# Performance work log

Measured on AMD Instinct MI355X. Metric: run time of the kernel, lower is better.

Reference implementation:

```python
import jax, jax.numpy as jnp
import numpy as np

N, E, D, H, ED = 50000, 150000, 128, 4, 16


def _ln(x, g, b, eps=1e-5):
    m = jnp.mean(x, -1, keepdims=True)
    v = jnp.var(x, -1, keepdims=True)
    return (x - m) / jnp.sqrt(v + eps) * g + b


def _seg_softmax(logits, seg, n):
    # numerically stable softmax over edges grouped by destination node
    m = jax.ops.segment_max(logits, seg, num_segments=n)
    e = jnp.exp(logits - m[seg])
    s = jax.ops.segment_sum(e, seg, num_segments=n)
    return e / (s[seg] + 1e-16)


def setup_inputs():
    key = jax.random.key(0)
    ks = jax.random.split(key, 16)
    def w(i, shape, s=0.05):
        return jax.random.normal(ks[i], shape, jnp.float32) * s
    return dict(
        x=w(0, (N, D), 1.0),
        edge_index=jax.random.randint(ks[1], (2, E), 0, N),
        edge_attr=w(2, (E, ED), 1.0),
        sage_Wl=w(3, (D, D)), sage_Wr=w(4, (D, D)), sage_b=jnp.zeros((D,), jnp.float32),
        tq_W=w(5, (D, H * D)), tq_b=jnp.zeros((H * D,), jnp.float32),
        tk_W=w(6, (D, H * D)), tk_b=jnp.zeros((H * D,), jnp.float32),
        tv_W=w(7, (D, H * D)), tv_b=jnp.zeros((H * D,), jnp.float32),
        te_W=w(8, (ED, H * D)),
        tskip_W=w(9, (D, D)), tskip_b=jnp.zeros((D,), jnp.float32),
        gat_W=w(10, (D, H * D)), gat_att_src=w(11, (H, D)), gat_att_dst=w(12, (H, D)),
        gat_bias=jnp.zeros((D,), jnp.float32),
        gate_short=jnp.ones((1,), jnp.float32), gate_attn=jnp.ones((1,), jnp.float32),
        gate_neighbor=jnp.ones((1,), jnp.float32),
        fus_W=w(13, (3 * D, D)), fus_b=jnp.zeros((D,), jnp.float32),
        fus_g=jnp.ones((D,), jnp.float32), fus_beta=jnp.zeros((D,), jnp.float32),
        norm_g=jnp.ones((D,), jnp.float32), norm_b=jnp.zeros((D,), jnp.float32),
    )


def reference(x, edge_index, edge_attr, sage_Wl, sage_Wr, sage_b,
              tq_W, tq_b, tk_W, tk_b, tv_W, tv_b, te_W, tskip_W, tskip_b,
              gat_W, gat_att_src, gat_att_dst, gat_bias,
              gate_short, gate_attn, gate_neighbor,
              fus_W, fus_b, fus_g, fus_beta, norm_g, norm_b):
    n, d = x.shape
    h = tq_W.shape[1] // d
    src, dst = edge_index[0], edge_index[1]

    # --- SAGEConv: mean aggregation of neighbors + root linear ---
    agg = jax.ops.segment_sum(x[src], dst, num_segments=n)
    cnt = jax.ops.segment_sum(jnp.ones((src.shape[0],), x.dtype), dst, num_segments=n)
    mean = agg / jnp.maximum(cnt, 1.0)[:, None]
    x_short = jax.nn.relu(mean @ sage_Wl + x @ sage_Wr + sage_b)

    # --- TransformerConv (concat=False, edge-conditioned key/value, skip) ---
    q = (x @ tq_W + tq_b).reshape(n, h, d)
    k = (x @ tk_W + tk_b).reshape(n, h, d)
    v = (x @ tv_W + tv_b).reshape(n, h, d)
    e = (edge_attr @ te_W).reshape(-1, h, d)           # [E,H,d]
    logits = jnp.sum(q[dst] * (k[src] + e), -1) / np.float32(np.sqrt(d))  # [E,H]
    alpha = _seg_softmax(logits, dst, n)
    out_t = jax.ops.segment_sum((v[src] + e) * alpha[..., None], dst, num_segments=n).mean(1)
    x_attn = jax.nn.relu(out_t + x @ tskip_W + tskip_b)

    # --- GATConv (adds self-loops, concat=False averages heads, bias) ---
    loops = jnp.arange(n)
    s2 = jnp.concatenate([src, loops])
    d2 = jnp.concatenate([dst, loops])
    g = (x @ gat_W).reshape(n, h, d)
    a_s = jnp.sum(g * gat_att_src, -1)                 # [N,H]
    a_d = jnp.sum(g * gat_att_dst, -1)
    lg = jax.nn.leaky_relu(a_s[s2] + a_d[d2], 0.2)     # [E+N,H]
    al = _seg_softmax(lg, d2, n)
    out_g = jax.ops.segment_sum(g[s2] * al[..., None], d2, num_segments=n).mean(1) + gat_bias
    x_nb = jax.nn.relu(out_g)

    # --- gated fusion + residual LayerNorm ---
    gs = jax.nn.sigmoid(gate_short)
    ga = jax.nn.sigmoid(gate_attn)
    gn = jax.nn.sigmoid(gate_neighbor)
    cat = jnp.concatenate([x_short * gs, x_attn * ga, x_nb * gn], -1)
    fused = jax.nn.relu(_ln(cat @ fus_W + fus_b, fus_g, fus_beta))
    return _ln(x + fused, norm_g, norm_b)
```

## Files before the change

kernel.cpp:

```cpp
#include <hip/hip_runtime.h>
#include <hip/hip_bf16.h>

using bf16 = __hip_bfloat16;
typedef __attribute__((ext_vector_type(8))) short short8;
typedef __attribute__((ext_vector_type(4))) float f32x4;
typedef __attribute__((ext_vector_type(4))) unsigned short u16x4;

__device__ __forceinline__ void store4(bf16* p, float v0, float v1, float v2, float v3) {
    u16x4 pk;
    bf16 h0 = __float2bfloat16(v0); pk[0] = *(unsigned short*)&h0;
    bf16 h1 = __float2bfloat16(v1); pk[1] = *(unsigned short*)&h1;
    bf16 h2 = __float2bfloat16(v2); pk[2] = *(unsigned short*)&h2;
    bf16 h3 = __float2bfloat16(v3); pk[3] = *(unsigned short*)&h3;
    *(u16x4*)p = pk;
}
__device__ __forceinline__ float b2f(short s) { bf16 h; *(short*)&h = s; return __bfloat162float(h); }

__global__ __launch_bounds__(256) void zero_ws(unsigned* p, size_t n) {
    size_t i = (size_t)blockIdx.x * 256 + threadIdx.x;
    size_t stride = (size_t)gridDim.x * 256;
    for (; i < n; i += stride) p[i] = 0u;
}

__global__ __launch_bounds__(256) void prep_all(
    const float* __restrict__ x, bf16* __restrict__ x_b,
    bf16* __restrict__ Wt_sage, const float* __restrict__ sage_Wl, const float* __restrict__ sage_Wr,
    bf16* __restrict__ Wt_fus, const float* __restrict__ fus_W,
    const float* __restrict__ gate_s, const float* __restrict__ gate_a, const float* __restrict__ gate_n,
    bf16* __restrict__ Wt_cat, const float* __restrict__ tvW,
    const float* __restrict__ tskipW, const float* __restrict__ teW,
    bf16* __restrict__ Wgag, const float* __restrict__ gatW,
    float* __restrict__ bvsum, const float* __restrict__ tvb, int ND)
{
    const int TP = 128 * 128;
    long i = (long)blockIdx.x * 256 + threadIdx.x;
    long nv = ND >> 3;
    if (i < nv) {
        long b = i * 8;
        f32x4 a0 = *(const f32x4*)(x + b);
        f32x4 a1 = *(const f32x4*)(x + b + 4);
        short8 o;
        #pragma unroll
        for (int j = 0; j < 4; ++j) { bf16 h = __float2bfloat16(a0[j]); o[j] = *(short*)&h; }
        #pragma unroll
        for (int j = 0; j < 4; ++j) { bf16 h = __float2bfloat16(a1[j]); o[4 + j] = *(short*)&h; }
        *(short8*)(x_b + b) = o;
        return;
    }
    i -= nv;
    if (i < TP) { int k = (int)i / 128, c = (int)i % 128; Wt_sage[c * 256 + k] = __float2bfloat16(sage_Wl[i]); return; }
    i -= TP;
    if (i < TP) { int k = (int)i / 128, c = (int)i % 128; Wt_sage[c * 256 + 128 + k] = __float2bfloat16(sage_Wr[i]); return; }
    i -= TP;
    if (i < 3 * TP) {
        int sseg = (int)(i / TP); int r = (int)(i % TP);
        int k = r / 128, c = r % 128;
        const float* g = sseg == 0 ? gate_s : (sseg == 1 ? gate_a : gate_n);
        float gv = 1.0f / (1.0f + expf(-g[0]));
        Wt_fus[c * 384 + sseg * 128 + k] = __float2bfloat16(fus_W[(size_t)sseg * TP + r] * gv);
        return;
    }
    i -= 3L * TP;
    if (i < 128L * 704) {
        int d = (int)(i / 704), kk = (int)(i % 704);
        float v;
        if (kk < 512)      { int h = kk >> 7, k = kk & 127; v = 0.25f * tvW[k * 512 + h * 128 + d]; }
        else if (kk < 640) { int k = kk - 512;              v = tskipW[k * 128 + d]; }
        else               { int t = kk - 640; int h = t >> 4, j = t & 15; v = 0.25f * teW[j * 512 + h * 128 + d]; }
        Wt_cat[(size_t)d * 704 + kk] = __float2bfloat16(v);
        return;
    }
    i -= 128L * 704;
    if (i < 128L * 512) {
        int d = (int)i >> 9, k = (int)i & 511;
        int h = k >> 7, i2 = k & 127;
        Wgag[i] = __float2bfloat16(0.25f * gatW[(size_t)i2 * 512 + h * 128 + d]);
        return;
    }
    i -= 128L * 512;
    if (i < 128) {
        int d = (int)i;
        bvsum[d] = 0.25f * (tvb[d] + tvb[128 + d] + tvb[256 + d] + tvb[384 + d]);
    }
}

__global__ __launch_bounds__(128) void build_wbig(
    bf16* __restrict__ Wbig, float* __restrict__ bbig,
    const float* __restrict__ Wq, const float* __restrict__ Wk,
    const float* __restrict__ teW, const float* __restrict__ bq,
    const float* __restrict__ bk, const float* __restrict__ gatW,
    const float* __restrict__ attS, const float* __restrict__ attD)
{
    int c = blockIdx.x;
    int ip = threadIdx.x;
    float acc = 0.f, bacc = 0.f;
    if (c < 512) {
        int h = c >> 7, i2 = c & 127;
        const float* wkrow = Wk + (size_t)i2 * 512 + h * 128;
        const float* wqrow = Wq + (size_t)ip * 512 + h * 128;
        for (int o = 0; o < 128; ++o) acc += wqrow[o] * wkrow[o];
        if (ip == 0) { const float* bqr = bq + h * 128; for (int o = 0; o < 128; ++o) bacc += bqr[o] * wkrow[o]; }
    } else if (c < 576) {
        int t = c - 512; int h = t >> 4, j = t & 15;
        const float* terow = teW + (size_t)j * 512 + h * 128;
        const float* wqrow = Wq + (size_t)ip * 512 + h * 128;
        for (int o = 0; o < 128; ++o) acc += wqrow[o] * terow[o];
        if (ip == 0) { const float* bqr = bq + h * 128; for (int o = 0; o < 128; ++o) bacc += bqr[o] * terow[o]; }
    } else if (c < 580) {
        int h = c - 576;
        const float* bkr = bk + h * 128;
        const float* wqrow = Wq + (size_t)ip * 512 + h * 128;
        for (int o = 0; o < 128; ++o) acc += wqrow[o] * bkr[o];
        if (ip == 0) { const float* bqr = bq + h * 128; for (int o = 0; o < 128; ++o) bacc += bqr[o] * bkr[o]; }
    } else if (c < 584) {
        int h = c - 580;
        const float* ar = attS + h * 128;
        const float* gr = gatW + (size_t)ip * 512 + h * 128;
        for (int d = 0; d < 128; ++d) acc += gr[d] * ar[d];
    } else if (c < 588) {
        int h = c - 584;
        const float* ar = attD + h * 128;
        const float* gr = gatW + (size_t)ip * 512 + h * 128;
        for (int d = 0; d < 128; ++d) acc += gr[d] * ar[d];
    }
    Wbig[(size_t)c * 128 + ip] = __float2bfloat16(acc);
    if (ip == 0) bbig[c] = bacc;
}

__global__ __launch_bounds__(256) void k_hist(const int* __restrict__ dst, int* __restrict__ deg_i, int E) {
    int e = blockIdx.x * 256 + threadIdx.x;
    if (e < E) atomicAdd(&deg_i[dst[e]], 1);
}

__global__ __launch_bounds__(256) void k_scan1(
    const int* __restrict__ deg_i, int* __restrict__ loc, int* __restrict__ partial, int N)
{
    __shared__ int sm[256];
    int t = threadIdx.x, i = blockIdx.x * 256 + t;
    int v = (i < N) ? deg_i[i] : 0;
    sm[t] = v;
    __syncthreads();
    for (int off = 1; off < 256; off <<= 1) {
        int add = (t >= off) ? sm[t - off] : 0;
        __syncthreads();
        sm[t] += add;
        __syncthreads();
    }
    if (i < N) loc[i] = sm[t] - v;
    if (t == 255) partial[blockIdx.x] = sm[255];
}

__global__ __launch_bounds__(256) void k_scan2(int* __restrict__ partial, int nb) {
    __shared__ int sm[256];
    int t = threadIdx.x;
    int v = (t < nb) ? partial[t] : 0;
    sm[t] = v;
    __syncthreads();
    for (int off = 1; off < 256; off <<= 1) {
        int add = (t >= off) ? sm[t - off] : 0;
        __syncthreads();
        sm[t] += add;
        __syncthreads();
    }
    if (t < nb) partial[t] = sm[t] - v;
}

__global__ __launch_bounds__(256) void k_scan3(
    const int* __restrict__ loc, const int* __restrict__ partial,
    int* __restrict__ rowptr, int* __restrict__ cursor, int N)
{
    int i = blockIdx.x * 256 + threadIdx.x;
    if (i >= N) return;
    int r = loc[i] + partial[blockIdx.x];
    rowptr[i] = r;
    cursor[i] = r;
}

__global__ __launch_bounds__(256) void k_scatter(
    const int* __restrict__ src, const int* __restrict__ dst,
    int* __restrict__ cursor, int* __restrict__ col_src, int* __restrict__ eidx, int E)
{
    int e = blockIdx.x * 256 + threadIdx.x;
    if (e >= E) return;
    int d = dst[e];
    int pos = atomicAdd(&cursor[d], 1);
    col_src[pos] = src[e];
    eidx[pos] = e;
}

__global__ __launch_bounds__(128) void gemm_wide(
    const bf16* __restrict__ A, const bf16* __restrict__ Wt,
    const float* __restrict__ bias, bf16* __restrict__ C, int n_rows, int ldc)
{
    int row0 = blockIdx.x * 64;
    int wave = threadIdx.x >> 6, lane = threadIdx.x & 63;
    int lrow = lane & 15, quad = lane >> 4;
    short8 xb[4][4];
    #pragma unroll
    for (int ks = 0; ks < 4; ++ks)
        #pragma unroll
        for (int nt = 0; nt < 4; ++nt) {
            int r = row0 + nt * 16 + lrow;
            r = r < n_rows ? r : n_rows - 1;
            xb[ks][nt] = *(const short8*)(A + (size_t)r * 128 + ks * 32 + quad * 8);
        }
    int cbase = blockIdx.y * 128 + wave * 64;
    f32x4 acc[4][4] = {};
    #pragma unroll
    for (int ks = 0; ks < 4; ++ks) {
        short8 wf[4];
        #pragma unroll
        for (int mt = 0; mt < 4; ++mt)
            wf[mt] = *(const short8*)(Wt + (size_t)(cbase + mt * 16 + lrow) * 128 + ks * 32 + quad * 8);
        #pragma unroll
        for (int mt = 0; mt < 4; ++mt)
            #pragma unroll
            for (int nt = 0; nt < 4; ++nt)
                acc[mt][nt] = __builtin_amdgcn_mfma_f32_16x16x32_bf16(wf[mt], xb[ks][nt], acc[mt][nt], 0, 0, 0);
    }
    #pragma unroll
    for (int nt = 0; nt < 4; ++nt) {
        int row = row0 + nt * 16 + lrow;
        if (row >= n_rows) continue;
        #pragma unroll
        for (int mt = 0; mt < 4; ++mt) {
            int col = cbase + mt * 16 + quad * 4;
            float b0 = 0.f, b1 = 0.f, b2 = 0.f, b3 = 0.f;
            if (bias) { b0 = bias[col]; b1 = bias[col + 1]; b2 = bias[col + 2]; b3 = bias[col + 3]; }
            store4(&C[(size_t)row * ldc + col],
                   acc[mt][nt][0] + b0, acc[mt][nt][1] + b1,
                   acc[mt][nt][2] + b2, acc[mt][nt][3] + b3);
        }
    }
}

#define NCAP 8
__global__ __launch_bounds__(256) void node_fused(
    const bf16* __restrict__ QT, const bf16* __restrict__ x_b,
    const float* __restrict__ edge_attr,
    const int* __restrict__ rowptr, const int* __restrict__ deg_i,
    const int* __restrict__ col_src, const int* __restrict__ eidx,
    bf16* __restrict__ mean_b, bf16* __restrict__ xa, bf16* __restrict__ ga,
    float* __restrict__ ea_agg, int N)
{
    __shared__ short8 xS[4][NCAP][16];
    __shared__ float eaS[4][NCAP][16];
    __shared__ float wTs[4][NCAP][4];
    __shared__ float wGs[4][NCAP][4];
    int w = threadIdx.x >> 6, l = threadIdx.x & 63;
    int n = blockIdx.x * 4 + w;
    if (n >= N) return;
    int j = l & 15, g4 = l >> 4;
    int p0 = rowptr[n], dg = deg_i[n];
    const float scale = 0.08838834764831845f;
    float qtF[4][8], qeqL[4], qbL[4], adh[4], ashn[4];
    #pragma unroll
    for (int h = 0; h < 4; ++h) {
        short8 q = *(const short8*)(QT + (size_t)n * 640 + h * 128 + j * 8);
        #pragma unroll
        for (int t = 0; t < 8; ++t) qtF[h][t] = b2f(q[t]);
        qeqL[h] = __bfloat162float(QT[(size_t)n * 640 + 512 + h * 16 + j]);
        qbL[h]  = __bfloat162float(QT[(size_t)n * 640 + 576 + h]);
        ashn[h] = __bfloat162float(QT[(size_t)n * 640 + 580 + h]);
        adh[h]  = __bfloat162float(QT[(size_t)n * 640 + 584 + h]);
    }
    float xn0 = __bfloat162float(x_b[(size_t)n * 128 + l]);
    float xn1 = __bfloat162float(x_b[(size_t)n * 128 + l + 64]);
    float s_t[4], s_g[4], xaacc[8] = {}, gaacc[8];
    float mean0 = 0.f, mean1 = 0.f, eaacc = 0.f;
    #pragma unroll
    for (int h = 0; h < 4; ++h) {
        s_t[h] = 0.f;
        float lgs = ashn[h] + adh[h];
        lgs = lgs > 0.f ? lgs : 0.2f * lgs;
        float e = __expf(lgs);
        s_g[h] = e;
        gaacc[h * 2] = e * xn0; gaacc[h * 2 + 1] = e * xn1;
    }
    for (int c0 = 0; c0 < dg; c0 += NCAP) {
        int cc = min(NCAP, dg - c0);
        for (int it = 0; it < ((cc + 3) >> 2); ++it) {
            int i = it * 4 + g4;
            bool valid = i < cc;
            int s = 0;
            short8 xf = {0, 0, 0, 0, 0, 0, 0, 0};
            float ea_j = 0.f;
            if (valid) {
                s = col_src[p0 + c0 + i];
                int eg = eidx[p0 + c0 + i];
                xf = *(const short8*)(x_b + (size_t)s * 128 + j * 8);
                ea_j = edge_attr[(size_t)eg * 16 + j];
                xS[w][i][j] = xf;
                eaS[w][i][j] = ea_j;
            }
            float xv[8];
            #pragma unroll
            for (int t = 0; t < 8; ++t) xv[t] = b2f(xf[t]);
            float p[4];
            #pragma unroll
            for (int h = 0; h < 4; ++h) {
                float a = ea_j * qeqL[h];
                #pragma unroll
                for (int t = 0; t < 8; ++t) a += xv[t] * qtF[h][t];
                p[h] = a;
            }
            #pragma unroll
            for (int off = 1; off < 16; off <<= 1)
                #pragma unroll
                for (int h = 0; h < 4; ++h)
                    p[h] += __shfl_xor(p[h], off, 64);
            if (valid && j == 0) {
                #pragma unroll
                for (int h = 0; h < 4; ++h) {
                    wTs[w][i][h] = __expf((p[h] + qbL[h]) * scale);
                    float as_s = __bfloat162float(QT[(size_t)s * 640 + 580 + h]);
                    float lg = as_s + adh[h];
                    lg = lg > 0.f ? lg : 0.2f * lg;
                    wGs[w][i][h] = __expf(lg);
                }
            }
        }
        for (int i = 0; i < cc; ++i) {
            const bf16* xr = (const bf16*)&xS[w][i][0];
            float xv0 = __bfloat162float(xr[l]);
            float xv1 = __bfloat162float(xr[l + 64]);
            mean0 += xv0; mean1 += xv1;
            #pragma unroll
            for (int h = 0; h < 4; ++h) {
                float at = wTs[w][i][h], ag = wGs[w][i][h];
                s_t[h] += at; s_g[h] += ag;
                xaacc[h * 2] += at * xv0; xaacc[h * 2 + 1] += at * xv1;
                gaacc[h * 2] += ag * xv0; gaacc[h * 2 + 1] += ag * xv1;
            }
            eaacc += wTs[w][i][g4] * eaS[w][i][j];
        }
    }
    float invd = 1.f / fmaxf((float)dg, 1.f);
    mean_b[(size_t)n * 128 + l]      = __float2bfloat16(mean0 * invd);
    mean_b[(size_t)n * 128 + l + 64] = __float2bfloat16(mean1 * invd);
    #pragma unroll
    for (int h = 0; h < 4; ++h) {
        float it = 1.f / (s_t[h] + 1e-16f);
        xa[(size_t)n * 512 + h * 128 + l]      = __float2bfloat16(xaacc[h * 2] * it);
        xa[(size_t)n * 512 + h * 128 + l + 64] = __float2bfloat16(xaacc[h * 2 + 1] * it);
        float ig = 1.f / (s_g[h] + 1e-16f);
        ga[(size_t)n * 512 + h * 128 + l]      = __float2bfloat16(gaacc[h * 2] * ig);
        ga[(size_t)n * 512 + h * 128 + l + 64] = __float2bfloat16(gaacc[h * 2 + 1] * ig);
    }
    ea_agg[(size_t)n * 64 + l] = eaacc / (s_t[g4] + 1e-16f);
}

#define MFMA_ACC(ACC) \
    _Pragma("unroll") \
    for (int mt = 0; mt < 4; ++mt) \
        _Pragma("unroll") \
        for (int nt = 0; nt < 4; ++nt) \
            ACC[mt][nt] = __builtin_amdgcn_mfma_f32_16x16x32_bf16(wf[mt], xf[nt], ACC[mt][nt], 0, 0, 0);

#define FUSE_SEG(SEG) do { \
    _Pragma("unroll") \
    for (int ks = 0; ks < 4; ++ks) { \
        int kT = ks * 32 + quad * 8; \
        short8 xf[4], wf[4]; \
        _Pragma("unroll") \
        for (int t = 0; t < 4; ++t) { \
            int row_l = t * 16 + lrow; \
            xf[t] = *(const short8*)(tileb + row_l * 256 + ((kT * 2) ^ ((row_l & 7) << 4))); \
            wf[t] = *(const short8*)(Wt_fus + (size_t)(cbase + t * 16 + lrow) * 384 + (SEG) * 128 + kT); \
        } \
        MFMA_ACC(facc) \
    } \
} while (0)

#define STASH(BIASP, USE_BV) do { \
    _Pragma("unroll") \
    for (int nt = 0; nt < 4; ++nt) { \
        int row_l = nt * 16 + lrow; \
        int sw = (row_l & 7) << 4; \
        float bvf = (USE_BV) ? ((deg_i[rA[nt]] > 0) ? 1.f : 0.f) : 0.f; \
        _Pragma("unroll") \
        for (int mt = 0; mt < 4; ++mt) { \
            int col = cbase + mt * 16 + quad * 4; \
            f32x4 bb = *(const f32x4*)((BIASP) + col); \
            u16x4 pk; \
            _Pragma("unroll") \
            for (int jj = 0; jj < 4; ++jj) { \
                float v = acc[mt][nt][jj] + bb[jj]; \
                if (USE_BV) v += bvf * bvsum[col + jj]; \
                bf16 h = __float2bfloat16(fmaxf(v, 0.f)); \
                pk[jj] = *(unsigned short*)&h; \
            } \
            *(u16x4*)(tileb + row_l * 256 + ((col * 2) ^ sw)) = pk; \
        } \
    } \
} while (0)

__global__ __launch_bounds__(128) void tail_fused(
    const bf16* __restrict__ mean_b, const bf16* __restrict__ x_b,
    const bf16* __restrict__ ga, const bf16* __restrict__ xa,
    const float* __restrict__ ea_agg, const int* __restrict__ deg_i,
    const float* __restrict__ x,
    const bf16* __restrict__ Wt_sage, const bf16* __restrict__ Wgag,
    const bf16* __restrict__ Wt_cat, const bf16* __restrict__ Wt_fus,
    const float* __restrict__ sage_b, const float* __restrict__ gat_bias,
    const float* __restrict__ tskip_b, const float* __restrict__ bvsum,
    const float* __restrict__ fus_b, const float* __restrict__ fus_g,
    const float* __restrict__ fus_beta, const float* __restrict__ norm_g,
    const float* __restrict__ norm_b,
    float* __restrict__ out, int N)
{
    __shared__ __align__(16) char tileb[64 * 256];
    __shared__ float2 st1[2][64];
    __shared__ float2 st2[2][64];
    int wave = threadIdx.x >> 6, lane = threadIdx.x & 63;
    int lrow = lane & 15, quad = lane >> 4;
    int row0 = blockIdx.x * 64;
    int cbase = wave * 64;
    int rA[4];
    #pragma unroll
    for (int t = 0; t < 4; ++t) {
        int r = row0 + t * 16 + lrow;
        rA[t] = r < N ? r : N - 1;
    }
    f32x4 facc[4][4] = {};

    {
        f32x4 acc[4][4] = {};
        for (int ks = 0; ks < 8; ++ks) {
            const bf16* A = (ks < 4) ? mean_b : x_b;
            int kA = (ks & 3) * 32 + quad * 8;
            int kW = ks * 32 + quad * 8;
            short8 xf[4], wf[4];
            #pragma unroll
            for (int t = 0; t < 4; ++t) {
                xf[t] = *(const short8*)(A + (size_t)rA[t] * 128 + kA);
                wf[t] = *(const short8*)(Wt_sage + (size_t)(cbase + t * 16 + lrow) * 256 + kW);
            }
            MFMA_ACC(acc)
        }
        STASH(sage_b, 0);
    }
    __syncthreads();
    FUSE_SEG(0);
    __syncthreads();

    {
        f32x4 acc[4][4] = {};
        for (int ks = 0; ks < 22; ++ks) {
            int kq = quad * 8;
            short8 xf[4], wf[4];
            #pragma unroll
            for (int t = 0; t < 4; ++t) {
                if (ks < 16) {
                    xf[t] = *(const short8*)(xa + (size_t)rA[t] * 512 + ks * 32 + kq);
                } else if (ks < 20) {
                    xf[t] = *(const short8*)(x_b + (size_t)rA[t] * 128 + (ks - 16) * 32 + kq);
                } else {
                    const float* ap = ea_agg + (size_t)rA[t] * 64 + (ks - 20) * 32 + kq;
                    f32x4 e0 = *(const f32x4*)(ap);
                    f32x4 e1 = *(const f32x4*)(ap + 4);
                    #pragma unroll
                    for (int jj = 0; jj < 4; ++jj) { bf16 hb = __float2bfloat16(e0[jj]); xf[t][jj] = *(short*)&hb; }
                    #pragma unroll
                    for (int jj = 0; jj < 4; ++jj) { bf16 hb = __float2bfloat16(e1[jj]); xf[t][4 + jj] = *(short*)&hb; }
                }
                wf[t] = *(const short8*)(Wt_cat + (size_t)(cbase + t * 16 + lrow) * 704 + ks * 32 + kq);
            }
            MFMA_ACC(acc)
        }
        STASH(tskip_b, 1);
    }
    __syncthreads();
    FUSE_SEG(1);
    __syncthreads();

    {
        f32x4 acc[4][4] = {};
        for (int ks = 0; ks < 16; ++ks) {
            int k = ks * 32 + quad * 8;
            short8 xf[4], wf[4];
            #pragma unroll
            for (int t = 0; t < 4; ++t) {
                xf[t] = *(const short8*)(ga + (size_t)rA[t] * 512 + k);
                wf[t] = *(const short8*)(Wgag + (size_t)(cbase + t * 16 + lrow) * 512 + k);
            }
            MFMA_ACC(acc)
        }
        STASH(gat_bias, 0);
    }
    __syncthreads();
    FUSE_SEG(2);

    #pragma unroll
    for (int nt = 0; nt < 4; ++nt) {
        float s = 0.f, q = 0.f;
        #pragma unroll
        for (int mt = 0; mt < 4; ++mt) {
            int col = cbase + mt * 16 + quad * 4;
            f32x4 bb = *(const f32x4*)(fus_b + col);
            #pragma unroll
            for (int jj = 0; jj < 4; ++jj) {
                float v = facc[mt][nt][jj] + bb[jj];
                facc[mt][nt][jj] = v;
                s += v; q += v * v;
            }
        }
        s += __shfl_xor(s, 16, 64); q += __shfl_xor(q, 16, 64);
        s += __shfl_xor(s, 32, 64); q += __shfl_xor(q, 32, 64);
        if (quad == 0) st1[wave][nt * 16 + lrow] = make_float2(s, q);
    }
    __syncthreads();
    float m1[4], inv1[4];
    #pragma unroll
    for (int nt = 0; nt < 4; ++nt) {
        float2 a = st1[0][nt * 16 + lrow], b = st1[1][nt * 16 + lrow];
        float S = a.x + b.x, Q = a.y + b.y;
        float m = S * (1.f / 128.f);
        m1[nt] = m;
        inv1[nt] = rsqrtf(Q * (1.f / 128.f) - m * m + 1e-5f);
    }
    #pragma unroll
    for (int nt = 0; nt < 4; ++nt) {
        float s = 0.f, q = 0.f;
        #pragma unroll
        for (int mt = 0; mt < 4; ++mt) {
            int col = cbase + mt * 16 + quad * 4;
            f32x4 gv = *(const f32x4*)(fus_g + col);
            f32x4 bv = *(const f32x4*)(fus_beta + col);
            f32x4 xv = *(const f32x4*)(x + (size_t)rA[nt] * 128 + col);
            #pragma unroll
            for (int jj = 0; jj < 4; ++jj) {
                float y = fmaxf((facc[mt][nt][jj] - m1[nt]) * inv1[nt] * gv[jj] + bv[jj], 0.f);
                float z = xv[jj] + y;
                facc[mt][nt][jj] = z;
                s += z; q += z * z;
            }
        }
        s += __shfl_xor(s, 16, 64); q += __shfl_xor(q, 16, 64);
        s += __shfl_xor(s, 32, 64); q += __shfl_xor(q, 32, 64);
        if (quad == 0) st2[wave][nt * 16 + lrow] = make_float2(s, q);
    }
    __syncthreads();
    #pragma unroll
    for (int nt = 0; nt < 4; ++nt) {
        int row = row0 + nt * 16 + lrow;
        if (row >= N) continue;
        float2 a = st2[0][nt * 16 + lrow], b = st2[1][nt * 16 + lrow];
        float S = a.x + b.x, Q = a.y + b.y;
        float m = S * (1.f / 128.f);
        float inv = rsqrtf(Q * (1.f / 128.f) - m * m + 1e-5f);
        #pragma unroll
        for (int mt = 0; mt < 4; ++mt) {
            int col = cbase + mt * 16 + quad * 4;
            f32x4 ngv = *(const f32x4*)(norm_g + col);
            f32x4 nbv = *(const f32x4*)(norm_b + col);
            f32x4 o;
            #pragma unroll
            for (int jj = 0; jj < 4; ++jj)
                o[jj] = (facc[mt][nt][jj] - m) * inv * ngv[jj] + nbv[jj];
            *(f32x4*)(out + (size_t)row * 128 + col) = o;
        }
    }
}

extern "C" void kernel_launch(void* const* d_in, const int* in_sizes, int n_in,
                              void* d_out, int out_size, void* d_ws, size_t ws_size,
                              hipStream_t stream)
{
    const float* x        = (const float*)d_in[0];
    const int*   ei       = (const int*)d_in[1];
    const float* edge_attr= (const float*)d_in[2];
    const float* sage_Wl  = (const float*)d_in[3];
    const float* sage_Wr  = (const float*)d_in[4];
    const float* sage_b   = (const float*)d_in[5];
    const float* tq_W     = (const float*)d_in[6];
    const float* tq_b     = (const float*)d_in[7];
    const float* tk_W     = (const float*)d_in[8];
    const float* tk_b     = (const float*)d_in[9];
    const float* tv_W     = (const float*)d_in[10];
    const float* tv_b     = (const float*)d_in[11];
    const float* te_W     = (const float*)d_in[12];
    const float* tskip_W  = (const float*)d_in[13];
    const float* tskip_b  = (const float*)d_in[14];
    const float* gat_W    = (const float*)d_in[15];
    const float* att_s_w  = (const float*)d_in[16];
    const float* att_d_w  = (const float*)d_in[17];
    const float* gat_bias = (const float*)d_in[18];
    const float* gate_s   = (const float*)d_in[19];
    const float* gate_a   = (const float*)d_in[20];
    const float* gate_n   = (const float*)d_in[21];
    const float* fus_W    = (const float*)d_in[22];
    const float* fus_b    = (const float*)d_in[23];
    const float* fus_g    = (const float*)d_in[24];
    const float* fus_beta = (const float*)d_in[25];
    const float* norm_g   = (const float*)d_in[26];
    const float* norm_b   = (const float*)d_in[27];

    int N = in_sizes[0] / 128;
    int E = in_sizes[2] / 16;
    const int* src = ei;
    const int* dst = ei + E;
    int ND = N * 128;
    int nb = (N + 255) / 256;

    char* wsb = (char*)d_ws;
    size_t off = 0;
    auto carve = [&](size_t bytes) -> char* {
        char* p = wsb + off;
        off += (bytes + 255) & ~(size_t)255;
        return p;
    };
    int*   deg_i   = (int*)carve((size_t)N * 4);
    size_t zero_bytes = off;
    int*   rowptr  = (int*)carve((size_t)N * 4);
    int*   cursor  = (int*)carve((size_t)N * 4);
    int*   loc     = (int*)carve((size_t)N * 4);
    int*   partial = (int*)carve((size_t)256 * 4);
    int*   col_src = (int*)carve((size_t)E * 4);
    int*   eidx    = (int*)carve((size_t)E * 4);
    bf16*  x_b     = (bf16*)carve((size_t)N * 128 * 2);
    bf16*  QT      = (bf16*)carve((size_t)N * 640 * 2);
    bf16*  xa      = (bf16*)carve((size_t)N * 512 * 2);
    bf16*  ga      = (bf16*)carve((size_t)N * 512 * 2);
    bf16*  mean_b  = (bf16*)carve((size_t)N * 128 * 2);
    float* ea_agg  = (float*)carve((size_t)N * 64 * 4);
    bf16*  Wbig    = (bf16*)carve((size_t)640 * 128 * 2);
    float* bbig    = (float*)carve((size_t)640 * 4);
    bf16*  Wt_sage = (bf16*)carve((size_t)128 * 256 * 2);
    bf16*  Wt_fus  = (bf16*)carve((size_t)128 * 384 * 2);
    bf16*  Wt_cat  = (bf16*)carve((size_t)128 * 704 * 2);
    bf16*  Wgag    = (bf16*)carve((size_t)128 * 512 * 2);
    float* bvsum   = (float*)carve((size_t)128 * 4);

    zero_ws<<<256, 256, 0, stream>>>((unsigned*)wsb, zero_bytes / 4);
    const long TP = 128 * 128;
    long prep_total = (long)(ND >> 3) + 5L * TP + 128L * 704 + 128L * 512 + 128;
    int prep_blocks = (int)((prep_total + 255) / 256);
    prep_all<<<prep_blocks, 256, 0, stream>>>(
        x, x_b, Wt_sage, sage_Wl, sage_Wr, Wt_fus, fus_W, gate_s, gate_a, gate_n,
        Wt_cat, tv_W, tskip_W, te_W, Wgag, gat_W, bvsum, tv_b, ND);
    build_wbig<<<640, 128, 0, stream>>>(Wbig, bbig, tq_W, tk_W, te_W, tq_b, tk_b,
                                        gat_W, att_s_w, att_d_w);

    k_hist<<<(E + 255) / 256, 256, 0, stream>>>(dst, deg_i, E);
    k_scan1<<<nb, 256, 0, stream>>>(deg_i, loc, partial, N);
    k_scan2<<<1, 256, 0, stream>>>(partial, nb);
    k_scan3<<<nb, 256, 0, stream>>>(loc, partial, rowptr, cursor, N);
    k_scatter<<<(E + 255) / 256, 256, 0, stream>>>(src, dst, cursor, col_src, eidx, E);

    int gy64 = (N + 63) / 64, gnode = (N + 3) / 4;

    gemm_wide<<<dim3(gy64, 5), 128, 0, stream>>>(x_b, Wbig, bbig, QT, N, 640);

    node_fused<<<gnode, 256, 0, stream>>>(QT, x_b, edge_attr, rowptr, deg_i, col_src, eidx,
                                          mean_b, xa, ga, ea_agg, N);

    tail_fused<<<gy64, 128, 0, stream>>>(
        mean_b, x_b, ga, xa, ea_agg, deg_i, x,
        Wt_sage, Wgag, Wt_cat, Wt_fus,
        sage_b, gat_bias, tskip_b, bvsum,
        fus_b, fus_g, fus_beta, norm_g, norm_b,
        (float*)d_out, N);
}
```

Measured before the change: 417.4 us.

## Pre-pack weights in MFMA fragment order and store edge aggregate as bf16

All transposed weight matrices (Wbig, Wt_sage, Wt_cat, Wgag, Wt_fus) are now written in a packed layout where each wave's 64 lanes read one contiguous 1 KB fragment per MFMA tile, instead of strided row loads. The aim is fully coalesced weight fetches in gemm_wide and tail_fused. Separately, the per-node edge-attribute aggregate is stored as bf16 rather than fp32, which halves its traffic and drops the in-loop conversion. The bf16 store adds a little rounding, but that value was already cast to bf16 before the MFMA, so the result should be unchanged.

Result: faster. 374.6 us (-10.3%).

```diff
diff --git a/kernel.cpp b/kernel.cpp
--- a/kernel.cpp
+++ b/kernel.cpp
@@ -15,6 +15,11 @@
     *(u16x4*)p = pk;
 }
 __device__ __forceinline__ float b2f(short s) { bf16 h; *(short*)&h = s; return __bfloat162float(h); }
+
+__device__ __forceinline__ size_t pidx(int c, int k, int K) {
+    return ((size_t)(((c >> 6) * (K >> 5) + (k >> 5)) * 4 + ((c >> 4) & 3)) * 64
+            + (((k >> 3) & 3) * 16 + (c & 15))) * 8 + (k & 7);
+}
 
 __global__ __launch_bounds__(256) void zero_ws(unsigned* p, size_t n) {
     size_t i = (size_t)blockIdx.x * 256 + threadIdx.x;
@@ -48,16 +53,16 @@
         return;
     }
     i -= nv;
-    if (i < TP) { int k = (int)i / 128, c = (int)i % 128; Wt_sage[c * 256 + k] = __float2bfloat16(sage_Wl[i]); return; }
+    if (i < TP) { int k = (int)i / 128, c = (int)i % 128; Wt_sage[pidx(c, k, 256)] = __float2bfloat16(sage_Wl[i]); return; }
     i -= TP;
-    if (i < TP) { int k = (int)i / 128, c = (int)i % 128; Wt_sage[c * 256 + 128 + k] = __float2bfloat16(sage_Wr[i]); return; }
+    if (i < TP) { int k = (int)i / 128, c = (int)i % 128; Wt_sage[pidx(c, k + 128, 256)] = __float2bfloat16(sage_Wr[i]); return; }
     i -= TP;
     if (i < 3 * TP) {
         int sseg = (int)(i / TP); int r = (int)(i % TP);
         int k = r / 128, c = r % 128;
         const float* g = sseg == 0 ? gate_s : (sseg == 1 ? gate_a : gate_n);
         float gv = 1.0f / (1.0f + expf(-g[0]));
-        Wt_fus[c * 384 + sseg * 128 + k] = __float2bfloat16(fus_W[(size_t)sseg * TP + r] * gv);
+        Wt_fus[pidx(c, sseg * 128 + k, 384)] = __float2bfloat16(fus_W[(size_t)sseg * TP + r] * gv);
         return;
     }
     i -= 3L * TP;
@@ -67,14 +72,14 @@
         if (kk < 512)      { int h = kk >> 7, k = kk & 127; v = 0.25f * tvW[k * 512 + h * 128 + d]; }
         else if (kk < 640) { int k = kk - 512;              v = tskipW[k * 128 + d]; }
         else               { int t = kk - 640; int h = t >> 4, j = t & 15; v = 0.25f * teW[j * 512 + h * 128 + d]; }
-        Wt_cat[(size_t)d * 704 + kk] = __float2bfloat16(v);
+        Wt_cat[pidx(d, kk, 704)] = __float2bfloat16(v);
         return;
     }
     i -= 128L * 704;
     if (i < 128L * 512) {
         int d = (int)i >> 9, k = (int)i & 511;
         int h = k >> 7, i2 = k & 127;
-        Wgag[i] = __float2bfloat16(0.25f * gatW[(size_t)i2 * 512 + h * 128 + d]);
+        Wgag[pidx(d, k, 512)] = __float2bfloat16(0.25f * gatW[(size_t)i2 * 512 + h * 128 + d]);
         return;
     }
     i -= 128L * 512;
@@ -123,7 +128,7 @@
         const float* gr = gatW + (size_t)ip * 512 + h * 128;
         for (int d = 0; d < 128; ++d) acc += gr[d] * ar[d];
     }
-    Wbig[(size_t)c * 128 + ip] = __float2bfloat16(acc);
+    Wbig[pidx(c, ip, 128)] = __float2bfloat16(acc);
     if (ip == 0) bbig[c] = bacc;
 }
 
@@ -204,14 +209,15 @@
             r = r < n_rows ? r : n_rows - 1;
             xb[ks][nt] = *(const short8*)(A + (size_t)r * 128 + ks * 32 + quad * 8);
         }
-    int cbase = blockIdx.y * 128 + wave * 64;
+    int c64 = blockIdx.y * 2 + wave;
+    int cbase = c64 * 64;
     f32x4 acc[4][4] = {};
     #pragma unroll
     for (int ks = 0; ks < 4; ++ks) {
         short8 wf[4];
         #pragma unroll
         for (int mt = 0; mt < 4; ++mt)
-            wf[mt] = *(const short8*)(Wt + (size_t)(cbase + mt * 16 + lrow) * 128 + ks * 32 + quad * 8);
+            wf[mt] = *(const short8*)(Wt + ((size_t)((c64 * 4 + ks) * 4 + mt) * 64 + lane) * 8);
         #pragma unroll
         for (int mt = 0; mt < 4; ++mt)
             #pragma unroll
@@ -241,7 +247,7 @@
     const int* __restrict__ rowptr, const int* __restrict__ deg_i,
     const int* __restrict__ col_src, const int* __restrict__ eidx,
     bf16* __restrict__ mean_b, bf16* __restrict__ xa, bf16* __restrict__ ga,
-    float* __restrict__ ea_agg, int N)
+    bf16* __restrict__ ea_b, int N)
 {
     __shared__ short8 xS[4][NCAP][16];
     __shared__ float eaS[4][NCAP][16];
@@ -347,7 +353,7 @@
         ga[(size_t)n * 512 + h * 128 + l]      = __float2bfloat16(gaacc[h * 2] * ig);
         ga[(size_t)n * 512 + h * 128 + l + 64] = __float2bfloat16(gaacc[h * 2 + 1] * ig);
     }
-    ea_agg[(size_t)n * 64 + l] = eaacc / (s_t[g4] + 1e-16f);
+    ea_b[(size_t)n * 64 + l] = __float2bfloat16(eaacc / (s_t[g4] + 1e-16f));
 }
 
 #define MFMA_ACC(ACC) \
@@ -366,8 +372,10 @@
         for (int t = 0; t < 4; ++t) { \
             int row_l = t * 16 + lrow; \
             xf[t] = *(const short8*)(tileb + row_l * 256 + ((kT * 2) ^ ((row_l & 7) << 4))); \
-            wf[t] = *(const short8*)(Wt_fus + (size_t)(cbase + t * 16 + lrow) * 384 + (SEG) * 128 + kT); \
         } \
+        _Pragma("unroll") \
+        for (int mt = 0; mt < 4; ++mt) \
+            wf[mt] = *(const short8*)(Wt_fus + ((size_t)((wave * 12 + (SEG) * 4 + ks) * 4 + mt) * 64 + lane) * 8); \
         MFMA_ACC(facc) \
     } \
 } while (0)
@@ -398,7 +406,7 @@
 __global__ __launch_bounds__(128) void tail_fused(
     const bf16* __restrict__ mean_b, const bf16* __restrict__ x_b,
     const bf16* __restrict__ ga, const bf16* __restrict__ xa,
-    const float* __restrict__ ea_agg, const int* __restrict__ deg_i,
+    const bf16* __restrict__ ea_b, const int* __restrict__ deg_i,
     const float* __restrict__ x,
     const bf16* __restrict__ Wt_sage, const bf16* __restrict__ Wgag,
     const bf16* __restrict__ Wt_cat, const bf16* __restrict__ Wt_fus,
@@ -429,13 +437,13 @@
         for (int ks = 0; ks < 8; ++ks) {
             const bf16* A = (ks < 4) ? mean_b : x_b;
             int kA = (ks & 3) * 32 + quad * 8;
-            int kW = ks * 32 + quad * 8;
             short8 xf[4], wf[4];
             #pragma unroll
-            for (int t = 0; t < 4; ++t) {
+            for (int t = 0; t < 4; ++t)
                 xf[t] = *(const short8*)(A + (size_t)rA[t] * 128 + kA);
-                wf[t] = *(const short8*)(Wt_sage + (size_t)(cbase + t * 16 + lrow) * 256 + kW);
-            }
+            #pragma unroll
+            for (int mt = 0; mt < 4; ++mt)
+                wf[mt] = *(const short8*)(Wt_sage + ((size_t)((wave * 8 + ks) * 4 + mt) * 64 + lane) * 8);
             MFMA_ACC(acc)
         }
         STASH(sage_b, 0);
@@ -456,16 +464,12 @@
                 } else if (ks < 20) {
                     xf[t] = *(const short8*)(x_b + (size_t)rA[t] * 128 + (ks - 16) * 32 + kq);
                 } else {
-                    const float* ap = ea_agg + (size_t)rA[t] * 64 + (ks - 20) * 32 + kq;
-                    f32x4 e0 = *(const f32x4*)(ap);
-                    f32x4 e1 = *(const f32x4*)(ap + 4);
-                    #pragma unroll
-                    for (int jj = 0; jj < 4; ++jj) { bf16 hb = __float2bfloat16(e0[jj]); xf[t][jj] = *(short*)&hb; }
-                    #pragma unroll
-                    for (int jj = 0; jj < 4; ++jj) { bf16 hb = __float2bfloat16(e1[jj]); xf[t][4 + jj] = *(short*)&hb; }
+                    xf[t] = *(const short8*)(ea_b + (size_t)rA[t] * 64 + (ks - 20) * 32 + kq);
                 }
-                wf[t] = *(const short8*)(Wt_cat + (size_t)(cbase + t * 16 + lrow) * 704 + ks * 32 + kq);
             }
+            #pragma unroll
+            for (int mt = 0; mt < 4; ++mt)
+                wf[mt] = *(const short8*)(Wt_cat + ((size_t)((wave * 22 + ks) * 4 + mt) * 64 + lane) * 8);
             MFMA_ACC(acc)
         }
         STASH(tskip_b, 1);
@@ -480,10 +484,11 @@
             int k = ks * 32 + quad * 8;
             short8 xf[4], wf[4];
             #pragma unroll
-            for (int t = 0; t < 4; ++t) {
+            for (int t = 0; t < 4; ++t)
                 xf[t] = *(const short8*)(ga + (size_t)rA[t] * 512 + k);
-                wf[t] = *(const short8*)(Wgag + (size_t)(cbase + t * 16 + lrow) * 512 + k);
-            }
+            #pragma unroll
+            for (int mt = 0; mt < 4; ++mt)
+                wf[mt] = *(const short8*)(Wgag + ((size_t)((wave * 16 + ks) * 4 + mt) * 64 + lane) * 8);
             MFMA_ACC(acc)
         }
         STASH(gat_bias, 0);
@@ -623,7 +628,7 @@
     bf16*  xa      = (bf16*)carve((size_t)N * 512 * 2);
     bf16*  ga      = (bf16*)carve((size_t)N * 512 * 2);
     bf16*  mean_b  = (bf16*)carve((size_t)N * 128 * 2);
-    float* ea_agg  = (float*)carve((size_t)N * 64 * 4);
+    bf16*  ea_b    = (bf16*)carve((size_t)N * 64 * 2);
     bf16*  Wbig    = (bf16*)carve((size_t)640 * 128 * 2);
     float* bbig    = (float*)carve((size_t)640 * 4);
     bf16*  Wt_sage = (bf16*)carve((size_t)128 * 256 * 2);
@@ -653,10 +658,10 @@
     gemm_wide<<<dim3(gy64, 5), 128, 0, stream>>>(x_b, Wbig, bbig, QT, N, 640);
 
     node_fused<<<gnode, 256, 0, stream>>>(QT, x_b, edge_attr, rowptr, deg_i, col_src, eidx,
-                                          mean_b, xa, ga, ea_agg, N);
+                                          mean_b, xa, ga, ea_b, N);
 
     tail_fused<<<gy64, 128, 0, stream>>>(
-        mean_b, x_b, ga, xa, ea_agg, deg_i, x,
+        mean_b, x_b, ga, xa, ea_b, deg_i, x,
         Wt_sage, Wgag, Wt_cat, Wt_fus,
         sage_b, gat_bias, tskip_b, bvsum,
         fus_b, fus_g, fus_beta, norm_g, norm_b,
```
